# Performance work log

Measured on AMD Instinct MI355X. Metric: run time of the kernel, lower is better.

Reference implementation:

```python
import jax, jax.numpy as jnp
import numpy as np
import math

N_NODES = 50000
N_EDGES = 400000
D = 256
H = 4
HD = D // H


def _layernorm(x, g, b, eps=1e-5):
    mu = jnp.mean(x, axis=-1, keepdims=True)
    var = jnp.mean((x - mu) ** 2, axis=-1, keepdims=True)
    return (x - mu) * jax.lax.rsqrt(var + eps) * g + b


def setup_inputs() -> dict:
    key = jax.random.key(0)
    ks = jax.random.split(key, 16)
    init = lambda k, sh: (jax.random.normal(k, sh, dtype=jnp.float32) * 0.02)
    inp = {
        "h_n": jax.random.normal(ks[0], (N_NODES, D), dtype=jnp.float32),
        "h_e": jax.random.normal(ks[1], (N_EDGES, D), dtype=jnp.float32),
        "edge_index": jax.random.randint(ks[2], (2, N_EDGES), 0, N_NODES, dtype=jnp.int64),
        "Wq_w": init(ks[3], (2 * D, D)), "Wq_b": jnp.zeros((D,), jnp.float32),
        "Wkv_w": init(ks[4], (2 * D, 2 * D)), "Wkv_b": jnp.zeros((2 * D,), jnp.float32),
        "Wo_w": init(ks[5], (D, D)), "Wo_b": jnp.zeros((D,), jnp.float32),
        "ln1_g": jnp.ones((D,), jnp.float32), "ln1_b": jnp.zeros((D,), jnp.float32),
        "ffn1_w": init(ks[6], (D, 4 * D)), "ffn1_b": jnp.zeros((4 * D,), jnp.float32),
        "ffn2_w": init(ks[7], (4 * D, D)), "ffn2_b": jnp.zeros((D,), jnp.float32),
        "ln2_g": jnp.ones((D,), jnp.float32), "ln2_b": jnp.zeros((D,), jnp.float32),
    }
    return inp


def reference(h_n, h_e, edge_index, Wq_w, Wq_b, Wkv_w, Wkv_b, Wo_w, Wo_b,
              ln1_g, ln1_b, ffn1_w, ffn1_b, ffn2_w, ffn2_b, ln2_g, ln2_b):
    num_nodes = h_n.shape[0]
    src, dst = edge_index[0], edge_index[1]

    # edge gathers
    q_input = jnp.concatenate([h_n[src], h_e], axis=-1)   # (E, 2D)
    kv_input = jnp.concatenate([h_n[dst], h_e], axis=-1)  # (E, 2D)

    Q = q_input @ Wq_w + Wq_b                             # (E, D)
    KV = kv_input @ Wkv_w + Wkv_b                         # (E, 2D)
    K, V = KV[:, :D], KV[:, D:]

    Q = Q.reshape(-1, H, HD)
    K = K.reshape(-1, H, HD)
    V = V.reshape(-1, H, HD)

    scores = jnp.sum(Q * K, axis=-1) / math.sqrt(HD)      # (E, H)

    # scatter softmax over edges grouped by src node
    m = jax.ops.segment_max(scores, src, num_segments=num_nodes)  # (N, H)
    ex = jnp.exp(scores - m[src])
    denom = jax.ops.segment_sum(ex, src, num_segments=num_nodes)  # (N, H)
    attn = ex / denom[src]                                        # (E, H)

    # scatter-sum of weighted values back to src nodes
    wv = attn[:, :, None] * V                                     # (E, H, HD)
    out = jax.ops.segment_sum(wv, src, num_segments=num_nodes)    # (N, H, HD)
    out = out.reshape(num_nodes, D)
    out = out @ Wo_w + Wo_b

    h = _layernorm(h_n + out, ln1_g, ln1_b)
    ff = jax.nn.gelu(h @ ffn1_w + ffn1_b, approximate=False) @ ffn2_w + ffn2_b
    h = _layernorm(h + ff, ln2_g, ln2_b)
    return h
```

## Files before the change

kernel.cpp:

```cpp
#include <hip/hip_runtime.h>
#include <hip/hip_bf16.h>
#include <cstdint>
#include <cstddef>


typedef __bf16 bf16;
typedef bf16 bf16x8 __attribute__((ext_vector_type(8)));
typedef bf16 bf16x4v __attribute__((ext_vector_type(4)));
typedef float f32x4 __attribute__((ext_vector_type(4)));
typedef const uint32_t __attribute__((address_space(1)))* gas_u32p;
typedef uint32_t __attribute__((address_space(3)))* las_u32p;

#define DEV static __device__ __forceinline__

static constexpr int NN = 50000;
static constexpr int NE = 400000;

DEV void async_copy16(const void* g, void* l) {
  __builtin_amdgcn_global_load_lds((gas_u32p)g, (las_u32p)l, 16, 0, 0);
}
DEV float bf2f(bf16 x) { return (float)x; }
DEV bf16  f2bf(float x) { return (bf16)x; }

template <int KV>
__global__ __launch_bounds__(256, 2) void gemm_edge(
    const bf16* __restrict__ hn, const bf16* __restrict__ he,
    const int* __restrict__ idx, const bf16* __restrict__ WT,
    const float* __restrict__ bias, const bf16* __restrict__ Qbf,
    bf16* __restrict__ outbf, float* __restrict__ scores) {
  __shared__ bf16 Al[128 * 32];
  __shared__ bf16 Bl[128 * 32];
  const int tid = threadIdx.x;
  const int e0 = blockIdx.x * 128;
  const int n0 = blockIdx.y * 128;

  const bf16* an[2];
  const bf16* ae[2];
  const bf16* bb[2];
#pragma unroll
  for (int p = 0; p < 2; ++p) {
    int c = tid + 256 * p;
    int row = c >> 2;
    int c8 = (c & 3) * 8;
    int e = e0 + row;
    int node = idx[e];
    an[p] = hn + (size_t)node * 256 + c8;
    ae[p] = he + (size_t)e * 256 + c8;
    bb[p] = WT + (size_t)(n0 + row) * 512 + c8;
  }

  const int wv = tid >> 6, lane = tid & 63;
  const int quad = lane >> 4, l16 = lane & 15;
  const int wrow = (wv >> 1) * 64, wcol = (wv & 1) * 64;

  f32x4 acc[4][4] = {};

  for (int k0 = 0; k0 < 512; k0 += 32) {
    if (k0) __syncthreads();
#pragma unroll
    for (int p = 0; p < 2; ++p) {
      const bf16* ga = (k0 < 256) ? (an[p] + k0) : (ae[p] + (k0 - 256));
      async_copy16(ga, &Al[(tid + 256 * p) * 8]);
      async_copy16(bb[p] + k0, &Bl[(tid + 256 * p) * 8]);
    }
    __syncthreads();
    bf16x8 af[4], bfr[4];
#pragma unroll
    for (int t = 0; t < 4; ++t)
      af[t] = *(const bf16x8*)&Al[(wrow + t * 16 + l16) * 32 + quad * 8];
#pragma unroll
    for (int t = 0; t < 4; ++t)
      bfr[t] = *(const bf16x8*)&Bl[(wcol + t * 16 + l16) * 32 + quad * 8];
#pragma unroll
    for (int mt = 0; mt < 4; ++mt)
#pragma unroll
      for (int nt = 0; nt < 4; ++nt)
        acc[mt][nt] = __builtin_amdgcn_mfma_f32_16x16x32_bf16(
            af[mt], bfr[nt], acc[mt][nt], 0, 0, 0);
  }

  if (KV == 0) {
#pragma unroll
    for (int nt = 0; nt < 4; ++nt) {
      int col = n0 + wcol + nt * 16 + l16;
      float bv = bias[col];
#pragma unroll
      for (int mt = 0; mt < 4; ++mt)
#pragma unroll
        for (int r = 0; r < 4; ++r) {
          int row = e0 + wrow + mt * 16 + quad * 4 + r;
          outbf[(size_t)row * 256 + col] = f2bf(acc[mt][nt][r] + bv);
        }
    }
  } else if (blockIdx.y < 2) {
    const int head = (n0 + wcol) >> 6;
    float bv[4];
#pragma unroll
    for (int nt = 0; nt < 4; ++nt) bv[nt] = bias[n0 + wcol + nt * 16 + l16];
#pragma unroll
    for (int mt = 0; mt < 4; ++mt)
#pragma unroll
      for (int r = 0; r < 4; ++r) {
        int row = e0 + wrow + mt * 16 + quad * 4 + r;
        float part = 0.f;
#pragma unroll
        for (int nt = 0; nt < 4; ++nt) {
          int col = n0 + wcol + nt * 16 + l16;
          part += (acc[mt][nt][r] + bv[nt]) * bf2f(Qbf[(size_t)row * 256 + col]);
        }
        part += __shfl_xor(part, 1);
        part += __shfl_xor(part, 2);
        part += __shfl_xor(part, 4);
        part += __shfl_xor(part, 8);
        if (l16 == 0) scores[(size_t)row * 4 + head] = part * 0.125f;
      }
  } else {
#pragma unroll
    for (int nt = 0; nt < 4; ++nt) {
      int col = n0 + wcol + nt * 16 + l16;
      float bv = bias[col];
#pragma unroll
      for (int mt = 0; mt < 4; ++mt)
#pragma unroll
        for (int r = 0; r < 4; ++r) {
          int row = e0 + wrow + mt * 16 + quad * 4 + r;
          outbf[(size_t)row * 256 + (col - 256)] = f2bf(acc[mt][nt][r] + bv);
        }
    }
  }
}

template <int KT, int EPI>
__global__ __launch_bounds__(256, 2) void gemm_node(
    const bf16* __restrict__ A, int M, const bf16* __restrict__ WT,
    const float* __restrict__ bias, int Nout, float* __restrict__ outf,
    bf16* __restrict__ outb) {
  __shared__ bf16 Al[128 * 32];
  __shared__ bf16 Bl[128 * 32];
  const int tid = threadIdx.x;
  const int m0 = blockIdx.x * 128;
  const int n0 = blockIdx.y * 128;
  const bf16* ab[2];
  const bf16* bb[2];
#pragma unroll
  for (int p = 0; p < 2; ++p) {
    int c = tid + 256 * p;
    int row = c >> 2;
    int c8 = (c & 3) * 8;
    int rg = m0 + row;
    if (rg > M - 1) rg = M - 1;
    ab[p] = A + (size_t)rg * KT + c8;
    bb[p] = WT + (size_t)(n0 + row) * KT + c8;
  }
  const int wv = tid >> 6, lane = tid & 63;
  const int quad = lane >> 4, l16 = lane & 15;
  const int wrow = (wv >> 1) * 64, wcol = (wv & 1) * 64;
  f32x4 acc[4][4] = {};
  for (int k0 = 0; k0 < KT; k0 += 32) {
    if (k0) __syncthreads();
#pragma unroll
    for (int p = 0; p < 2; ++p) {
      async_copy16(ab[p] + k0, &Al[(tid + 256 * p) * 8]);
      async_copy16(bb[p] + k0, &Bl[(tid + 256 * p) * 8]);
    }
    __syncthreads();
    bf16x8 af[4], bfr[4];
#pragma unroll
    for (int t = 0; t < 4; ++t)
      af[t] = *(const bf16x8*)&Al[(wrow + t * 16 + l16) * 32 + quad * 8];
#pragma unroll
    for (int t = 0; t < 4; ++t)
      bfr[t] = *(const bf16x8*)&Bl[(wcol + t * 16 + l16) * 32 + quad * 8];
#pragma unroll
    for (int mt = 0; mt < 4; ++mt)
#pragma unroll
      for (int nt = 0; nt < 4; ++nt)
        acc[mt][nt] = __builtin_amdgcn_mfma_f32_16x16x32_bf16(
            af[mt], bfr[nt], acc[mt][nt], 0, 0, 0);
  }
#pragma unroll
  for (int nt = 0; nt < 4; ++nt) {
    int col = n0 + wcol + nt * 16 + l16;
    float bv = bias[col];
#pragma unroll
    for (int mt = 0; mt < 4; ++mt)
#pragma unroll
      for (int r = 0; r < 4; ++r) {
        int row = m0 + wrow + mt * 16 + quad * 4 + r;
        if (row < M) {
          float v = acc[mt][nt][r] + bv;
          if (EPI == 0)
            outf[(size_t)row * Nout + col] = v;
          else
            outb[(size_t)row * Nout + col] =
                f2bf(0.5f * v * (1.f + erff(v * 0.70710678118654752f)));
        }
      }
  }
}

__global__ __launch_bounds__(256) void cast_bf16(const float* __restrict__ in,
                                                 bf16* __restrict__ out, int n) {
  int i = (blockIdx.x * 256 + threadIdx.x) * 4;
  if (i < n) {
    float4 v = *(const float4*)(in + i);
    bf16x4v o = {f2bf(v.x), f2bf(v.y), f2bf(v.z), f2bf(v.w)};
    *(bf16x4v*)(out + i) = o;
  }
}

__global__ __launch_bounds__(256) void transpose_cast(
    const float* __restrict__ W, bf16* __restrict__ WT, int K, int N) {
  int i = blockIdx.x * 256 + threadIdx.x;
  if (i < K * N) {
    int k = i / N, n = i - k * N;
    WT[(size_t)n * K + k] = f2bf(W[i]);
  }
}

__global__ __launch_bounds__(256) void count_deg(const int* __restrict__ src,
                                                 int* __restrict__ deg, int nE) {
  int e = blockIdx.x * 256 + threadIdx.x;
  if (e < nE) atomicAdd(&deg[src[e]], 1);
}

__global__ __launch_bounds__(256) void scan_offs(const int* __restrict__ deg,
                                                 int* __restrict__ offs,
                                                 int* __restrict__ cursor,
                                                 int nN) {
  __shared__ int part[256];
  int tid = threadIdx.x;
  int per = (nN + 255) >> 8;
  int lo = tid * per, hi = lo + per;
  if (hi > nN) hi = nN;
  int sm = 0;
  for (int i = lo; i < hi; ++i) sm += deg[i];
  part[tid] = sm;
  __syncthreads();
  if (tid == 0) {
    int run = 0;
    for (int i = 0; i < 256; ++i) {
      int v = part[i];
      part[i] = run;
      run += v;
    }
  }
  __syncthreads();
  int run = part[tid];
  for (int i = lo; i < hi; ++i) {
    offs[i] = run;
    cursor[i] = run;
    run += deg[i];
  }
  if (tid == 255) offs[nN] = run;
}

__global__ __launch_bounds__(256) void scatter_edges(const int* __restrict__ src,
                                                     int* __restrict__ cursor,
                                                     int* __restrict__ eperm,
                                                     int nE) {
  int e = blockIdx.x * 256 + threadIdx.x;
  if (e < nE) {
    int p = atomicAdd(&cursor[src[e]], 1);
    eperm[p] = e;
  }
}

__global__ __launch_bounds__(256) void aggregate(
    const int* __restrict__ offs, const int* __restrict__ eperm,
    const float* __restrict__ scores, const bf16* __restrict__ Vbf,
    bf16* __restrict__ outbf) {
  int n = blockIdx.x;
  int s = offs[n];
  int deg = offs[n + 1] - s;
  int tid = threadIdx.x, wv = tid >> 6, lane = tid & 63;
  __shared__ float mdl[4], dnl[4];
  float mx = -3.4e38f;
  for (int i = lane; i < deg; i += 64) {
    int e = eperm[s + i];
    mx = fmaxf(mx, scores[(size_t)e * 4 + wv]);
  }
#pragma unroll
  for (int o = 32; o; o >>= 1) mx = fmaxf(mx, __shfl_xor(mx, o));
  float sm = 0.f;
  for (int i = lane; i < deg; i += 64) {
    int e = eperm[s + i];
    sm += expf(scores[(size_t)e * 4 + wv] - mx);
  }
#pragma unroll
  for (int o = 32; o; o >>= 1) sm += __shfl_xor(sm, o);
  if (lane == 0) {
    mdl[wv] = mx;
    dnl[wv] = sm;
  }
  __syncthreads();
  int c = tid, h = tid >> 6;
  float m = mdl[h];
  float rd = dnl[h] > 0.f ? 1.f / dnl[h] : 0.f;
  float acc = 0.f;
  for (int i = 0; i < deg; ++i) {
    int e = eperm[s + i];
    float w = expf(scores[(size_t)e * 4 + h] - m) * rd;
    acc += w * bf2f(Vbf[(size_t)e * 256 + c]);
  }
  outbf[(size_t)n * 256 + c] = f2bf(acc);
}

__global__ __launch_bounds__(256) void ln_kernel(
    const float* __restrict__ x1, const float* __restrict__ x2,
    const float* __restrict__ g, const float* __restrict__ b,
    float* __restrict__ outf, bf16* __restrict__ outb) {
  int n = blockIdx.x, tid = threadIdx.x;
  float x = x1[(size_t)n * 256 + tid] + x2[(size_t)n * 256 + tid];
  float s = x, s2 = x * x;
#pragma unroll
  for (int o = 32; o; o >>= 1) {
    s += __shfl_xor(s, o);
    s2 += __shfl_xor(s2, o);
  }
  __shared__ float ls[4], ls2[4];
  int wv = tid >> 6, lane = tid & 63;
  if (lane == 0) {
    ls[wv] = s;
    ls2[wv] = s2;
  }
  __syncthreads();
  s = ls[0] + ls[1] + ls[2] + ls[3];
  s2 = ls2[0] + ls2[1] + ls2[2] + ls2[3];
  float mu = s * (1.f / 256.f);
  float var = s2 * (1.f / 256.f) - mu * mu;
  float y = (x - mu) * rsqrtf(var + 1e-5f) * g[tid] + b[tid];
  if (outf) outf[(size_t)n * 256 + tid] = y;
  if (outb) outb[(size_t)n * 256 + tid] = f2bf(y);
}

static constexpr size_t OFF_HN = 0;
static constexpr size_t OFF_HE = OFF_HN + 25600000;
static constexpr size_t OFF_WQT = OFF_HE + 204800000;
static constexpr size_t OFF_WKVT = OFF_WQT + 262144;
static constexpr size_t OFF_WOT = OFF_WKVT + 524288;
static constexpr size_t OFF_W1T = OFF_WOT + 131072;
static constexpr size_t OFF_W2T = OFF_W1T + 524288;
static constexpr size_t OFF_SC = OFF_W2T + 524288;
static constexpr size_t OFF_DEG = OFF_SC + 6400000;
static constexpr size_t OFF_OFFS = OFF_DEG + 200000;
static constexpr size_t OFF_CUR = OFF_OFFS + 200064;
static constexpr size_t OFF_EPERM = OFF_CUR + 200000;
static constexpr size_t OFF_AOUT = OFF_EPERM + 1600000;
static constexpr size_t OFF_Q = OFF_AOUT + 25600000;
static constexpr size_t OFF_V = OFF_Q + 204800000;
static constexpr size_t OFF_TMP = OFF_Q;
static constexpr size_t OFF_H1F = OFF_Q + 51200000;
static constexpr size_t OFF_H1B = OFF_Q + 102400000;
static constexpr size_t OFF_TMP2 = OFF_Q + 128000000;
static constexpr size_t OFF_FFM = OFF_HE;

extern "C" void kernel_launch(void* const* d_in, const int* in_sizes, int n_in,
                              void* d_out, int out_size, void* d_ws,
                              size_t ws_size, hipStream_t stream) {
  const float* h_n = (const float*)d_in[0];
  const float* h_e = (const float*)d_in[1];
  const int* eidx = (const int*)d_in[2];
  const int* src = eidx;
  const int* dst = eidx + NE;
  const float* Wq_w = (const float*)d_in[3];
  const float* Wq_b = (const float*)d_in[4];
  const float* Wkv_w = (const float*)d_in[5];
  const float* Wkv_b = (const float*)d_in[6];
  const float* Wo_w = (const float*)d_in[7];
  const float* Wo_b = (const float*)d_in[8];
  const float* ln1_g = (const float*)d_in[9];
  const float* ln1_b = (const float*)d_in[10];
  const float* f1_w = (const float*)d_in[11];
  const float* f1_b = (const float*)d_in[12];
  const float* f2_w = (const float*)d_in[13];
  const float* f2_b = (const float*)d_in[14];
  const float* ln2_g = (const float*)d_in[15];
  const float* ln2_b = (const float*)d_in[16];

  uint8_t* ws = (uint8_t*)d_ws;
  bf16* hn_bf = (bf16*)(ws + OFF_HN);
  bf16* he_bf = (bf16*)(ws + OFF_HE);
  bf16* WqT = (bf16*)(ws + OFF_WQT);
  bf16* WkvT = (bf16*)(ws + OFF_WKVT);
  bf16* WoT = (bf16*)(ws + OFF_WOT);
  bf16* W1T = (bf16*)(ws + OFF_W1T);
  bf16* W2T = (bf16*)(ws + OFF_W2T);
  float* scores = (float*)(ws + OFF_SC);
  int* deg = (int*)(ws + OFF_DEG);
  int* offs = (int*)(ws + OFF_OFFS);
  int* cursor = (int*)(ws + OFF_CUR);
  int* eperm = (int*)(ws + OFF_EPERM);
  bf16* aout = (bf16*)(ws + OFF_AOUT);
  bf16* Qbf = (bf16*)(ws + OFF_Q);
  bf16* Vbf = (bf16*)(ws + OFF_V);
  float* tmp = (float*)(ws + OFF_TMP);
  float* h1f = (float*)(ws + OFF_H1F);
  bf16* h1b = (bf16*)(ws + OFF_H1B);
  float* tmp2 = (float*)(ws + OFF_TMP2);
  bf16* ffm = (bf16*)(ws + OFF_FFM);

  cast_bf16<<<12500, 256, 0, stream>>>(h_n, hn_bf, NN * 256);
  cast_bf16<<<100000, 256, 0, stream>>>(h_e, he_bf, NE * 256);
  transpose_cast<<<512, 256, 0, stream>>>(Wq_w, WqT, 512, 256);
  transpose_cast<<<1024, 256, 0, stream>>>(Wkv_w, WkvT, 512, 512);
  transpose_cast<<<256, 256, 0, stream>>>(Wo_w, WoT, 256, 256);
  transpose_cast<<<1024, 256, 0, stream>>>(f1_w, W1T, 256, 1024);
  transpose_cast<<<1024, 256, 0, stream>>>(f2_w, W2T, 1024, 256);

  hipMemsetAsync(deg, 0, NN * sizeof(int), stream);
  count_deg<<<1563, 256, 0, stream>>>(src, deg, NE);
  scan_offs<<<1, 256, 0, stream>>>(deg, offs, cursor, NN);
  scatter_edges<<<1563, 256, 0, stream>>>(src, cursor, eperm, NE);

  gemm_edge<0><<<dim3(3125, 2), 256, 0, stream>>>(hn_bf, he_bf, src, WqT, Wq_b,
                                                  nullptr, Qbf, nullptr);
  gemm_edge<1><<<dim3(3125, 4), 256, 0, stream>>>(hn_bf, he_bf, dst, WkvT,
                                                  Wkv_b, Qbf, Vbf, scores);

  aggregate<<<NN, 256, 0, stream>>>(offs, eperm, scores, Vbf, aout);

  gemm_node<256, 0><<<dim3(391, 2), 256, 0, stream>>>(aout, NN, WoT, Wo_b, 256,
                                                      tmp, nullptr);
  ln_kernel<<<NN, 256, 0, stream>>>(h_n, tmp, ln1_g, ln1_b, h1f, h1b);

  gemm_node<256, 1><<<dim3(391, 8), 256, 0, stream>>>(h1b, NN, W1T, f1_b, 1024,
                                                      nullptr, ffm);
  gemm_node<1024, 0><<<dim3(391, 2), 256, 0, stream>>>(ffm, NN, W2T, f2_b, 256,
                                                       tmp2, nullptr);
  ln_kernel<<<NN, 256, 0, stream>>>(h1f, tmp2, ln2_g, ln2_b, (float*)d_out,
                                    nullptr);
}
```

Before: 1.896 ms.

## Double-buffer GEMM LDS tiles, swizzle LDS layout, and swap grid axes for reuse

Both edge and node GEMM kernels now double-buffer the A/B LDS tiles, issuing the next k-step's async global-to-LDS copies before computing the current one. They synchronise with explicit vmcnt waits and raw barriers. The LDS layout is XOR-swizzled on the 8-element column chunks to reduce bank conflicts on the fragment reads. The grid axes are swapped so blocks sharing the same row tile (the gathered edge/node rows) run adjacently, which should improve L2 reuse of A. Doubling LDS per block may reduce occupancy, and the hand-written waitcnt logic relies on the compiler not reordering other memory operations.

```diff
diff --git a/kernel.cpp b/kernel.cpp
--- a/kernel.cpp
+++ b/kernel.cpp
@@ -22,17 +22,23 @@
 DEV float bf2f(bf16 x) { return (float)x; }
 DEV bf16  f2bf(float x) { return (bf16)x; }
 
+DEV void raw_barrier() { __asm volatile("s_barrier" ::: "memory"); }
+DEV void wait_vm4() { __asm volatile("s_waitcnt vmcnt(4)" ::: "memory"); }
+DEV void wait_vm0() { __asm volatile("s_waitcnt vmcnt(0)" ::: "memory"); }
+
+DEV int stage_off(int c) { return (((c & 3) ^ ((c >> 3) & 3)) * 8); }
+
 template <int KV>
 __global__ __launch_bounds__(256, 2) void gemm_edge(
     const bf16* __restrict__ hn, const bf16* __restrict__ he,
     const int* __restrict__ idx, const bf16* __restrict__ WT,
     const float* __restrict__ bias, const bf16* __restrict__ Qbf,
     bf16* __restrict__ outbf, float* __restrict__ scores) {
-  __shared__ bf16 Al[128 * 32];
-  __shared__ bf16 Bl[128 * 32];
+  __shared__ bf16 Al[2][128 * 32];
+  __shared__ bf16 Bl[2][128 * 32];
   const int tid = threadIdx.x;
-  const int e0 = blockIdx.x * 128;
-  const int n0 = blockIdx.y * 128;
+  const int n0 = blockIdx.x * 128;
+  const int e0 = blockIdx.y * 128;
 
   const bf16* an[2];
   const bf16* ae[2];
@@ -41,7 +47,7 @@
   for (int p = 0; p < 2; ++p) {
     int c = tid + 256 * p;
     int row = c >> 2;
-    int c8 = (c & 3) * 8;
+    int c8 = stage_off(c);
     int e = e0 + row;
     int node = idx[e];
     an[p] = hn + (size_t)node * 256 + c8;
@@ -52,31 +58,44 @@
   const int wv = tid >> 6, lane = tid & 63;
   const int quad = lane >> 4, l16 = lane & 15;
   const int wrow = (wv >> 1) * 64, wcol = (wv & 1) * 64;
+  const int swz = (l16 >> 1) & 3;
+  const int aoff = (quad ^ swz) * 8;
 
   f32x4 acc[4][4] = {};
 
-  for (int k0 = 0; k0 < 512; k0 += 32) {
-    if (k0) __syncthreads();
+  auto issue = [&](int k0, int buf) {
 #pragma unroll
     for (int p = 0; p < 2; ++p) {
       const bf16* ga = (k0 < 256) ? (an[p] + k0) : (ae[p] + (k0 - 256));
-      async_copy16(ga, &Al[(tid + 256 * p) * 8]);
-      async_copy16(bb[p] + k0, &Bl[(tid + 256 * p) * 8]);
-    }
-    __syncthreads();
+      async_copy16(ga, &Al[buf][(tid + 256 * p) * 8]);
+      async_copy16(bb[p] + k0, &Bl[buf][(tid + 256 * p) * 8]);
+    }
+  };
+
+  issue(0, 0);
+  for (int s = 0; s < 16; ++s) {
+    const int cur = s & 1;
+    if (s < 15) {
+      issue((s + 1) * 32, cur ^ 1);
+      wait_vm4();
+    } else {
+      wait_vm0();
+    }
+    raw_barrier();
     bf16x8 af[4], bfr[4];
 #pragma unroll
     for (int t = 0; t < 4; ++t)
-      af[t] = *(const bf16x8*)&Al[(wrow + t * 16 + l16) * 32 + quad * 8];
+      af[t] = *(const bf16x8*)&Al[cur][(wrow + t * 16 + l16) * 32 + aoff];
 #pragma unroll
     for (int t = 0; t < 4; ++t)
-      bfr[t] = *(const bf16x8*)&Bl[(wcol + t * 16 + l16) * 32 + quad * 8];
+      bfr[t] = *(const bf16x8*)&Bl[cur][(wcol + t * 16 + l16) * 32 + aoff];
 #pragma unroll
     for (int mt = 0; mt < 4; ++mt)
 #pragma unroll
       for (int nt = 0; nt < 4; ++nt)
         acc[mt][nt] = __builtin_amdgcn_mfma_f32_16x16x32_bf16(
             af[mt], bfr[nt], acc[mt][nt], 0, 0, 0);
+    raw_barrier();
   }
 
   if (KV == 0) {
@@ -92,7 +111,7 @@
           outbf[(size_t)row * 256 + col] = f2bf(acc[mt][nt][r] + bv);
         }
     }
-  } else if (blockIdx.y < 2) {
+  } else if (n0 < 256) {
     const int head = (n0 + wcol) >> 6;
     float bv[4];
 #pragma unroll
@@ -135,18 +154,18 @@
     const bf16* __restrict__ A, int M, const bf16* __restrict__ WT,
     const float* __restrict__ bias, int Nout, float* __restrict__ outf,
     bf16* __restrict__ outb) {
-  __shared__ bf16 Al[128 * 32];
-  __shared__ bf16 Bl[128 * 32];
+  __shared__ bf16 Al[2][128 * 32];
+  __shared__ bf16 Bl[2][128 * 32];
   const int tid = threadIdx.x;
-  const int m0 = blockIdx.x * 128;
-  const int n0 = blockIdx.y * 128;
+  const int n0 = blockIdx.x * 128;
+  const int m0 = blockIdx.y * 128;
   const bf16* ab[2];
   const bf16* bb[2];
 #pragma unroll
   for (int p = 0; p < 2; ++p) {
     int c = tid + 256 * p;
     int row = c >> 2;
-    int c8 = (c & 3) * 8;
+    int c8 = stage_off(c);
     int rg = m0 + row;
     if (rg > M - 1) rg = M - 1;
     ab[p] = A + (size_t)rg * KT + c8;
@@ -155,28 +174,43 @@
   const int wv = tid >> 6, lane = tid & 63;
   const int quad = lane >> 4, l16 = lane & 15;
   const int wrow = (wv >> 1) * 64, wcol = (wv & 1) * 64;
+  const int swz = (l16 >> 1) & 3;
+  const int aoff = (quad ^ swz) * 8;
   f32x4 acc[4][4] = {};
-  for (int k0 = 0; k0 < KT; k0 += 32) {
-    if (k0) __syncthreads();
+
+  auto issue = [&](int k0, int buf) {
 #pragma unroll
     for (int p = 0; p < 2; ++p) {
-      async_copy16(ab[p] + k0, &Al[(tid + 256 * p) * 8]);
-      async_copy16(bb[p] + k0, &Bl[(tid + 256 * p) * 8]);
-    }
-    __syncthreads();
+      async_copy16(ab[p] + k0, &Al[buf][(tid + 256 * p) * 8]);
+      async_copy16(bb[p] + k0, &Bl[buf][(tid + 256 * p) * 8]);
+    }
+  };
+
+  constexpr int NSTEP = KT / 32;
+  issue(0, 0);
+  for (int s = 0; s < NSTEP; ++s) {
+    const int cur = s & 1;
+    if (s < NSTEP - 1) {
+      issue((s + 1) * 32, cur ^ 1);
+      wait_vm4();
+    } else {
+      wait_vm0();
+    }
+    raw_barrier();
     bf16x8 af[4], bfr[4];
 #pragma unroll
     for (int t = 0; t < 4; ++t)
-      af[t] = *(const bf16x8*)&Al[(wrow + t * 16 + l16) * 32 + quad * 8];
+      af[t] = *(const bf16x8*)&Al[cur][(wrow + t * 16 + l16) * 32 + aoff];
 #pragma unroll
     for (int t = 0; t < 4; ++t)
-      bfr[t] = *(const bf16x8*)&Bl[(wcol + t * 16 + l16) * 32 + quad * 8];
+      bfr[t] = *(const bf16x8*)&Bl[cur][(wcol + t * 16 + l16) * 32 + aoff];
 #pragma unroll
     for (int mt = 0; mt < 4; ++mt)
 #pragma unroll
       for (int nt = 0; nt < 4; ++nt)
         acc[mt][nt] = __builtin_amdgcn_mfma_f32_16x16x32_bf16(
             af[mt], bfr[nt], acc[mt][nt], 0, 0, 0);
+    raw_barrier();
   }
 #pragma unroll
   for (int nt = 0; nt < 4; ++nt) {
@@ -413,20 +447,20 @@
   scan_offs<<<1, 256, 0, stream>>>(deg, offs, cursor, NN);
   scatter_edges<<<1563, 256, 0, stream>>>(src, cursor, eperm, NE);
 
-  gemm_edge<0><<<dim3(3125, 2), 256, 0, stream>>>(hn_bf, he_bf, src, WqT, Wq_b,
+  gemm_edge<0><<<dim3(2, 3125), 256, 0, stream>>>(hn_bf, he_bf, src, WqT, Wq_b,
                                                   nullptr, Qbf, nullptr);
-  gemm_edge<1><<<dim3(3125, 4), 256, 0, stream>>>(hn_bf, he_bf, dst, WkvT,
+  gemm_edge<1><<<dim3(4, 3125), 256, 0, stream>>>(hn_bf, he_bf, dst, WkvT,
                                                   Wkv_b, Qbf, Vbf, scores);
 
   aggregate<<<NN, 256, 0, stream>>>(offs, eperm, scores, Vbf, aout);
 
-  gemm_node<256, 0><<<dim3(391, 2), 256, 0, stream>>>(aout, NN, WoT, Wo_b, 256,
+  gemm_node<256, 0><<<dim3(2, 391), 256, 0, stream>>>(aout, NN, WoT, Wo_b, 256,
                                                       tmp, nullptr);
   ln_kernel<<<NN, 256, 0, stream>>>(h_n, tmp, ln1_g, ln1_b, h1f, h1b);
 
-  gemm_node<256, 1><<<dim3(391, 8), 256, 0, stream>>>(h1b, NN, W1T, f1_b, 1024,
+  gemm_node<256, 1><<<dim3(8, 391), 256, 0, stream>>>(h1b, NN, W1T, f1_b, 1024,
                                                       nullptr, ffm);
-  gemm_node<1024, 0><<<dim3(391, 2), 256, 0, stream>>>(ffm, NN, W2T, f2_b, 256,
+  gemm_node<1024, 0><<<dim3(2, 391), 256, 0, stream>>>(ffm, NN, W2T, f2_b, 256,
                                                        tmp2, nullptr);
   ln_kernel<<<NN, 256, 0, stream>>>(h1f, tmp2, ln2_g, ln2_b, (float*)d_out,
                                     nullptr);
```

Measured after the change: 1.896 ms. About the same (+0.0%).
